# Kernel optimization log

Hardware: AMD Instinct MI355X
Metric: run time of the kernel (lower is better)

Reference implementation:

```python
import jax, jax.numpy as jnp
import numpy as np

B, L, D, K, C = 4, 1024, 1024, 20, 21  # images, proposals/img, feat dim, dict size, classes


def setup_inputs() -> dict:
    key = jax.random.key(0)
    ks = jax.random.split(key, 6)
    return {
        "x": jax.random.normal(ks[0], (B, L, D), jnp.float32),
        "dic": jax.random.normal(ks[1], (K, D), jnp.float32),
        "prior": jax.random.uniform(ks[2], (K,), jnp.float32),
        "Wy_w": jax.random.normal(ks[3], (C, D), jnp.float32) * 0.02,
        "Wy_b": jnp.zeros((C,), jnp.float32),
        "Wz_w": jax.random.normal(ks[4], (C, D), jnp.float32) * 0.02,
        "Wz_b": jnp.zeros((C,), jnp.float32),
        "cs_w": jax.random.normal(ks[5], (C, 2 * D), jnp.float32) * 0.01,
        "cs_b": jnp.zeros((C,), jnp.float32),
    }


def reference(x, dic, prior, Wy_w, Wy_b, Wz_w, Wz_b, cs_w, cs_b):
    # attention over a small class dictionary, then pairwise outer-sum causal logits.
    scale = 1.0 / jnp.sqrt(jnp.asarray(C, x.dtype))  # embedding_size ** 0.5 == sqrt(21)
    zd = dic @ Wz_w.T + Wz_b  # [K, C] Wz(dic), shared across images

    def per_image(y):  # y: [L, D]
        att = jax.nn.softmax(((y @ Wy_w.T + Wy_b) @ zd.T) * scale, axis=1)  # [L, K]
        # prior @ (att[:, :, None] * dic[None]) == (att * prior) @ dic
        z = (att * prior[None, :]) @ dic  # [L, D]
        # causal_score(cat(y_i, z_j)) == y_i @ W[:, :D].T + z_j @ W[:, D:].T + b
        ly = y @ cs_w[:, :D].T            # [L, C]
        lz = z @ cs_w[:, D:].T + cs_b     # [L, C]
        return (ly[:, None, :] + lz[None, :, :]).reshape(L * L, C)  # [L*L, C]

    return jax.vmap(per_image)(x)  # [B, L*L, C]
```

## Files before the change

kernel.cpp:

```cpp
#include <hip/hip_runtime.h>
#include <math.h>

#define BB 4
#define LL 1024
#define DD 1024
#define KK 20
#define CC 21
#define LC (LL * CC)
#define NQ (LC / 4)

typedef float vf4   __attribute__((ext_vector_type(4)));
typedef short bf16x8 __attribute__((ext_vector_type(8)));
typedef float f32x4  __attribute__((ext_vector_type(4)));

__device__ __forceinline__ unsigned short f2bf(float f) {
    unsigned int u = __builtin_bit_cast(unsigned int, f);
    u += 0x7FFFu + ((u >> 16) & 1u);
    return (unsigned short)(u >> 16);
}

__device__ __forceinline__ float wave_reduce_sum(float v) {
    #pragma unroll
    for (int off = 1; off < 64; off <<= 1)
        v += __shfl_xor(v, off, 64);
    return v;
}

__global__ __launch_bounds__(64) void k0_zdM(
    const float* __restrict__ dic,
    const float* __restrict__ Wz_w, const float* __restrict__ Wz_b,
    const float* __restrict__ cs_w, const float* __restrict__ Wy_w,
    float* __restrict__ zd, float* __restrict__ M,
    unsigned short* __restrict__ Wcat)
{
    int blk = blockIdx.x;
    int lane = threadIdx.x;

    if (blk < 2 * KK * CC) {
        bool isM = (blk >= KK * CC);
        int e2 = isM ? blk - KK * CC : blk;
        int k = e2 / CC, c = e2 % CC;
        const float* a = dic + k * DD;
        const float* w = isM ? (cs_w + (size_t)c * (2 * DD) + DD) : (Wz_w + c * DD);
        float p = 0.f;
        #pragma unroll
        for (int i = 0; i < DD / 64; ++i) {
            int d = lane + 64 * i;
            p += a[d] * w[d];
        }
        p = wave_reduce_sum(p);
        if (lane == 0) {
            if (isM) M[e2] = p;
            else     zd[e2] = p + Wz_b[c];
        }
    } else {
        int e2 = blk - 2 * KK * CC;
        int base = e2 * 2048;
        #pragma unroll
        for (int t = 0; t < 32; ++t) {
            int i = base + lane + 64 * t;
            int c = i >> 10, k = i & 1023;
            float v;
            if (c < CC)          v = Wy_w[(size_t)c * DD + k];
            else if (c < 2 * CC) v = cs_w[(size_t)(c - CC) * (2 * DD) + k];
            else                 v = 0.f;
            Wcat[i] = f2bf(v);
        }
    }
}

__global__ __launch_bounds__(256) void k1_mfma(
    const float* __restrict__ x,
    const float* __restrict__ prior,
    const float* __restrict__ Wy_b, const float* __restrict__ cs_b,
    const unsigned short* __restrict__ Wcat,
    const float* __restrict__ zd, const float* __restrict__ M,
    float* __restrict__ ly_ws, float* __restrict__ lz_ws)
{
    const int tid  = threadIdx.x;
    const int wid  = tid >> 6;
    const int lane = tid & 63;
    const int fr   = lane & 15;
    const int kg   = lane >> 4;
    const int r0   = blockIdx.x * 16;

    __shared__ float zds[KK * CC];
    __shared__ float Ms[KK * CC];
    __shared__ float pr[KK];
    __shared__ float bias[2 * CC];
    __shared__ float pacc[4 * 16 * 49];

    for (int i = tid; i < KK * CC; i += 256) { zds[i] = zd[i]; Ms[i] = M[i]; }
    if (tid < KK) pr[tid] = prior[tid];
    if (tid < CC) { bias[tid] = Wy_b[tid]; bias[CC + tid] = cs_b[tid]; }

    const int kbase = wid * 256;
    const float*          xp  = x    + (size_t)(r0 + fr) * DD + kbase + kg * 8;
    const unsigned short* w0p = Wcat + (size_t)(fr +  0) * DD + kbase + kg * 8;
    const unsigned short* w1p = Wcat + (size_t)(fr + 16) * DD + kbase + kg * 8;
    const unsigned short* w2p = Wcat + (size_t)(fr + 32) * DD + kbase + kg * 8;

    f32x4 acc0 = {0.f, 0.f, 0.f, 0.f};
    f32x4 acc1 = {0.f, 0.f, 0.f, 0.f};
    f32x4 acc2 = {0.f, 0.f, 0.f, 0.f};

    #pragma unroll
    for (int ks = 0; ks < 8; ++ks) {
        float4 a0 = *reinterpret_cast<const float4*>(xp + ks * 32);
        float4 a1 = *reinterpret_cast<const float4*>(xp + ks * 32 + 4);
        bf16x8 af;
        af[0] = (short)f2bf(a0.x); af[1] = (short)f2bf(a0.y);
        af[2] = (short)f2bf(a0.z); af[3] = (short)f2bf(a0.w);
        af[4] = (short)f2bf(a1.x); af[5] = (short)f2bf(a1.y);
        af[6] = (short)f2bf(a1.z); af[7] = (short)f2bf(a1.w);
        bf16x8 b0 = *reinterpret_cast<const bf16x8*>(w0p + ks * 32);
        bf16x8 b1 = *reinterpret_cast<const bf16x8*>(w1p + ks * 32);
        bf16x8 b2 = *reinterpret_cast<const bf16x8*>(w2p + ks * 32);
        acc0 = __builtin_amdgcn_mfma_f32_16x16x32_bf16(af, b0, acc0, 0, 0, 0);
        acc1 = __builtin_amdgcn_mfma_f32_16x16x32_bf16(af, b1, acc1, 0, 0, 0);
        acc2 = __builtin_amdgcn_mfma_f32_16x16x32_bf16(af, b2, acc2, 0, 0, 0);
    }

    #pragma unroll
    for (int j = 0; j < 4; ++j) {
        float* pw = pacc + (wid * 16 + kg * 4 + j) * 49;
        pw[fr]      = acc0[j];
        pw[16 + fr] = acc1[j];
        pw[32 + fr] = acc2[j];
    }
    __syncthreads();

    #pragma unroll
    for (int p = 0; p < 3; ++p) {
        int o = tid + p * 256;
        int row = o / 48, col = o % 48;
        float s = pacc[row * 49 + col]
                + pacc[(16 + row) * 49 + col]
                + pacc[(32 + row) * 49 + col]
                + pacc[(48 + row) * 49 + col];
        pacc[row * 49 + col] = s;
    }
    __syncthreads();

    if (tid < 64) {
        const float* f = pacc + fr * 49;
        const float scale = 0.21821789023599238f;
        float s[KK];
        float m = -1e30f;
        #pragma unroll
        for (int k = 0; k < KK; ++k) {
            float t = 0.f;
            #pragma unroll
            for (int c = 0; c < CC; ++c) t += (f[c] + bias[c]) * zds[k * CC + c];
            s[k] = t * scale;
            m = fmaxf(m, s[k]);
        }
        float sum = 0.f;
        #pragma unroll
        for (int k = 0; k < KK; ++k) { s[k] = expf(s[k] - m); sum += s[k]; }
        float inv = 1.f / sum;
        float wk[KK];
        #pragma unroll
        for (int k = 0; k < KK; ++k) wk[k] = s[k] * inv * pr[k];

        size_t rr = (size_t)(r0 + fr);
        for (int c = kg; c < CC; c += 4) {
            float lzv = bias[CC + c];
            #pragma unroll
            for (int k = 0; k < KK; ++k) lzv += wk[k] * Ms[k * CC + c];
            ly_ws[rr * CC + c] = f[CC + c];
            lz_ws[rr * CC + c] = lzv;
        }
    }
}

__global__ __launch_bounds__(512) void k2_outer(
    const float* __restrict__ ly_ws, const float* __restrict__ lz_ws,
    float* __restrict__ out)
{
    int tid = threadIdx.x;
    int blk = blockIdx.x;
    int b  = blk >> 8;
    int i0 = (blk & 255) << 2;

    __shared__ vf4 lyp4[4 * CC];
    {
        float* lyp = reinterpret_cast<float*>(lyp4);
        if (tid < 4 * 84) {
            int i = tid / 84, f = tid % 84;
            lyp[i * 84 + f] = ly_ws[(size_t)(b * LL + i0 + i) * CC + (f % 21)];
        }
    }

    const float* lzp = lz_ws + (size_t)b * LC;
    vf4 lzv[11];
    #pragma unroll
    for (int it = 0; it < 11; ++it) {
        int idx = tid + it * 512;
        if (idx < NQ) {
            lzv[it] = *reinterpret_cast<const vf4*>(lzp + (size_t)idx * 4);
        } else {
            lzv[it] = (vf4){0.f, 0.f, 0.f, 0.f};
        }
    }
    __syncthreads();

    int g0 = tid % 21;

    #pragma unroll
    for (int i = 0; i < 4; ++i) {
        float* op = out + (size_t)(b * LL + i0 + i) * LC;
        const vf4* lyp_i = lyp4 + i * CC;
        int g = g0;
        #pragma unroll
        for (int it = 0; it < 11; ++it) {
            int idx = tid + it * 512;
            if (idx < NQ) {
                *reinterpret_cast<vf4*>(op + (size_t)idx * 4) = lzv[it] + lyp_i[g];
            }
            g += 8; if (g >= 21) g -= 21;
        }
    }
}

extern "C" void kernel_launch(void* const* d_in, const int* in_sizes, int n_in,
                              void* d_out, int out_size, void* d_ws, size_t ws_size,
                              hipStream_t stream)
{
    const float* x     = (const float*)d_in[0];
    const float* dic   = (const float*)d_in[1];
    const float* prior = (const float*)d_in[2];
    const float* Wy_w  = (const float*)d_in[3];
    const float* Wy_b  = (const float*)d_in[4];
    const float* Wz_w  = (const float*)d_in[5];
    const float* Wz_b  = (const float*)d_in[6];
    const float* cs_w  = (const float*)d_in[7];
    const float* cs_b  = (const float*)d_in[8];
    float* out = (float*)d_out;

    float* ws = (float*)d_ws;
    float* zd = ws;
    float* M  = ws + 512;
    float* ly = ws + 1024;
    float* lz = ly + BB * LL * CC;
    unsigned short* Wcat = (unsigned short*)(ws + 1024 + 2 * BB * LL * CC);

    k0_zdM <<<dim3(2 * KK * CC + 24), dim3(64),  0, stream>>>(dic, Wz_w, Wz_b, cs_w, Wy_w,
                                                              zd, M, Wcat);
    k1_mfma<<<dim3(BB * LL / 16),     dim3(256), 0, stream>>>(x, prior, Wy_b, cs_b, Wcat,
                                                              zd, M, ly, lz);
    k2_outer<<<dim3(BB * LL / 4),     dim3(512), 0, stream>>>(ly, lz, out);
}
```

Measured before the change: 103.6 us.

## Stage x tile through LDS as bf16 with coalesced loads and split K over 8 waves

k1 now loads each 16-row x tile with fully coalesced float4 reads, converts it to bf16 and stores it in a padded shared-memory buffer. The MFMA loop then reads its A fragments from shared memory. The block grows to 512 threads so each of 8 waves handles 128 of the K dimension, and the partial-sum reduction runs over 8 waves. This targets the strided global loads in k1, at the cost of about 33KB more LDS per block, which lowers occupancy. k2, which writes the large output and likely dominates total time, is unchanged.

```diff
diff --git a/kernel.cpp b/kernel.cpp
--- a/kernel.cpp
+++ b/kernel.cpp
@@ -8,8 +8,9 @@
 #define CC 21
 #define LC (LL * CC)
 #define NQ (LC / 4)
-
-typedef float vf4   __attribute__((ext_vector_type(4)));
+#define XSTRIDE 1032
+
+typedef float vf4    __attribute__((ext_vector_type(4)));
 typedef short bf16x8 __attribute__((ext_vector_type(8)));
 typedef float f32x4  __attribute__((ext_vector_type(4)));
 
@@ -69,7 +70,7 @@
     }
 }
 
-__global__ __launch_bounds__(256) void k1_mfma(
+__global__ __launch_bounds__(512) void k1_mfma(
     const float* __restrict__ x,
     const float* __restrict__ prior,
     const float* __restrict__ Wy_b, const float* __restrict__ cs_b,
@@ -88,31 +89,38 @@
     __shared__ float Ms[KK * CC];
     __shared__ float pr[KK];
     __shared__ float bias[2 * CC];
-    __shared__ float pacc[4 * 16 * 49];
-
-    for (int i = tid; i < KK * CC; i += 256) { zds[i] = zd[i]; Ms[i] = M[i]; }
+    __shared__ float pacc[8 * 16 * 49];
+    __shared__ unsigned short xT[16 * XSTRIDE];
+
+    for (int i = tid; i < KK * CC; i += 512) { zds[i] = zd[i]; Ms[i] = M[i]; }
     if (tid < KK) pr[tid] = prior[tid];
     if (tid < CC) { bias[tid] = Wy_b[tid]; bias[CC + tid] = cs_b[tid]; }
 
-    const int kbase = wid * 256;
-    const float*          xp  = x    + (size_t)(r0 + fr) * DD + kbase + kg * 8;
+    #pragma unroll
+    for (int i = 0; i < 8; ++i) {
+        int f = tid + i * 512;
+        int row  = f >> 8;
+        int col4 = f & 255;
+        float4 v = *reinterpret_cast<const float4*>(x + (size_t)(r0 + row) * DD + col4 * 4);
+        unsigned int lo = (unsigned int)f2bf(v.x) | ((unsigned int)f2bf(v.y) << 16);
+        unsigned int hi = (unsigned int)f2bf(v.z) | ((unsigned int)f2bf(v.w) << 16);
+        *reinterpret_cast<uint2*>(&xT[row * XSTRIDE + col4 * 4]) = make_uint2(lo, hi);
+    }
+    __syncthreads();
+
+    const int kbase = wid * 128;
     const unsigned short* w0p = Wcat + (size_t)(fr +  0) * DD + kbase + kg * 8;
     const unsigned short* w1p = Wcat + (size_t)(fr + 16) * DD + kbase + kg * 8;
     const unsigned short* w2p = Wcat + (size_t)(fr + 32) * DD + kbase + kg * 8;
+    const unsigned short* ap  = xT + fr * XSTRIDE + kbase + kg * 8;
 
     f32x4 acc0 = {0.f, 0.f, 0.f, 0.f};
     f32x4 acc1 = {0.f, 0.f, 0.f, 0.f};
     f32x4 acc2 = {0.f, 0.f, 0.f, 0.f};
 
     #pragma unroll
-    for (int ks = 0; ks < 8; ++ks) {
-        float4 a0 = *reinterpret_cast<const float4*>(xp + ks * 32);
-        float4 a1 = *reinterpret_cast<const float4*>(xp + ks * 32 + 4);
-        bf16x8 af;
-        af[0] = (short)f2bf(a0.x); af[1] = (short)f2bf(a0.y);
-        af[2] = (short)f2bf(a0.z); af[3] = (short)f2bf(a0.w);
-        af[4] = (short)f2bf(a1.x); af[5] = (short)f2bf(a1.y);
-        af[6] = (short)f2bf(a1.z); af[7] = (short)f2bf(a1.w);
+    for (int ks = 0; ks < 4; ++ks) {
+        bf16x8 af = *reinterpret_cast<const bf16x8*>(ap + ks * 32);
         bf16x8 b0 = *reinterpret_cast<const bf16x8*>(w0p + ks * 32);
         bf16x8 b1 = *reinterpret_cast<const bf16x8*>(w1p + ks * 32);
         bf16x8 b2 = *reinterpret_cast<const bf16x8*>(w2p + ks * 32);
@@ -123,7 +131,7 @@
 
     #pragma unroll
     for (int j = 0; j < 4; ++j) {
-        float* pw = pacc + (wid * 16 + kg * 4 + j) * 49;
+        float* pw = pacc + ((wid * 16) + kg * 4 + j) * 49;
         pw[fr]      = acc0[j];
         pw[16 + fr] = acc1[j];
         pw[32 + fr] = acc2[j];
@@ -131,14 +139,15 @@
     __syncthreads();
 
     #pragma unroll
-    for (int p = 0; p < 3; ++p) {
-        int o = tid + p * 256;
-        int row = o / 48, col = o % 48;
-        float s = pacc[row * 49 + col]
-                + pacc[(16 + row) * 49 + col]
-                + pacc[(32 + row) * 49 + col]
-                + pacc[(48 + row) * 49 + col];
-        pacc[row * 49 + col] = s;
+    for (int p = 0; p < 2; ++p) {
+        int o = tid + p * 512;
+        if (o < 768) {
+            int row = o / 48, col = o % 48;
+            float s = 0.f;
+            #pragma unroll
+            for (int w = 0; w < 8; ++w) s += pacc[((w * 16) + row) * 49 + col];
+            pacc[row * 49 + col] = s;
+        }
     }
     __syncthreads();
 
@@ -191,20 +200,15 @@
             lyp[i * 84 + f] = ly_ws[(size_t)(b * LL + i0 + i) * CC + (f % 21)];
         }
     }
-
     const float* lzp = lz_ws + (size_t)b * LC;
     vf4 lzv[11];
     #pragma unroll
     for (int it = 0; it < 11; ++it) {
         int idx = tid + it * 512;
-        if (idx < NQ) {
-            lzv[it] = *reinterpret_cast<const vf4*>(lzp + (size_t)idx * 4);
-        } else {
-            lzv[it] = (vf4){0.f, 0.f, 0.f, 0.f};
-        }
-    }
-    __syncthreads();
-
+        lzv[it] = (idx < NQ) ? *reinterpret_cast<const vf4*>(lzp + (size_t)idx * 4)
+                             : (vf4){0.f, 0.f, 0.f, 0.f};
+    }
+    __syncthreads();
     int g0 = tid % 21;
 
     #pragma unroll
@@ -247,7 +251,7 @@
 
     k0_zdM <<<dim3(2 * KK * CC + 24), dim3(64),  0, stream>>>(dic, Wz_w, Wz_b, cs_w, Wy_w,
                                                               zd, M, Wcat);
-    k1_mfma<<<dim3(BB * LL / 16),     dim3(256), 0, stream>>>(x, prior, Wy_b, cs_b, Wcat,
+    k1_mfma<<<dim3(BB * LL / 16),     dim3(512), 0, stream>>>(x, prior, Wy_b, cs_b, Wcat,
                                                               zd, M, ly, lz);
     k2_outer<<<dim3(BB * LL / 4),     dim3(512), 0, stream>>>(ly, lz, out);
 }
```

New measurement: 99.54 us. 3.9% less time.
